# Optimization experiments

Measured on AMD Instinct MI355X. Metric: run time of the kernel, lower is better.

## Reference

```python
import jax, jax.numpy as jnp
import numpy as np

EPS = 1e-10
COMMITMENT_COST = 0.25


def setup_inputs() -> dict:
    key = jax.random.key(0)
    kx, kw = jax.random.split(key)
    B, H, W, D, K = 32, 32, 32, 256, 8192
    x = jax.random.normal(kx, (B, H, W, D), dtype=jnp.float32)
    # codebook initialized RandomUniform(-1, 1), shape [embedding_dim, n_embeddings]
    w = jax.random.uniform(kw, (D, K), dtype=jnp.float32, minval=-1.0, maxval=1.0)
    return {"x": x, "w": w, "is_training": 1}


def reference(x, w, is_training):
    D, K = w.shape
    flat_x = x.reshape(-1, D)  # [N, D]
    distances = (
        jnp.sum(flat_x * flat_x, axis=1, keepdims=True)
        - 2.0 * (flat_x @ w)
        + jnp.sum(w * w, axis=0, keepdims=True)
    )
    encoding_indices_flat = jnp.argmin(distances, axis=1)  # [N]
    encodings = jax.nn.one_hot(encoding_indices_flat, K, dtype=x.dtype)  # [N, K]
    encoding_indices = encoding_indices_flat.reshape(x.shape[:-1])  # [B, H, W]
    quantized = jnp.take(w.T, encoding_indices, axis=0)  # [B, H, W, D]

    e_latent_loss = jnp.mean((jax.lax.stop_gradient(quantized) - x) ** 2)
    q_latent_loss = jnp.mean((quantized - jax.lax.stop_gradient(x)) ** 2)
    loss = q_latent_loss + COMMITMENT_COST * e_latent_loss

    # straight-through estimator
    quantized_st = x + jax.lax.stop_gradient(quantized - x)

    avg_probs = jnp.mean(encodings, axis=0)  # [K]
    perplexity = jnp.exp(-jnp.sum(avg_probs * jnp.log(avg_probs + EPS)))

    return quantized_st, loss, perplexity, encodings, encoding_indices
```

## Files before the change

kernel.cpp:

```cpp
#include <hip/hip_runtime.h>
#include <math.h>

typedef _Float16 f16x8 __attribute__((ext_vector_type(8)));
typedef float f32x4 __attribute__((ext_vector_type(4)));

#define N_PTS 32768
#define DIM 256
#define K_CODES 8192
#define NSTRIP 4

#define WS_WNH     0
#define WS_COUNTS  32768
#define WS_LOSSP   65536
#define WS_PART    262144
#define WS_WT      2359296
#define WS_BPK     10747904

#define GLL(dst, src) __builtin_amdgcn_global_load_lds( \
    (const __attribute__((address_space(1))) void*)(src), \
    (__attribute__((address_space(3))) void*)(dst), 16, 0, 0)

__global__ void vq_prep(const float* __restrict__ w, float* __restrict__ wnh,
                        int* __restrict__ counts) {
    int k = blockIdx.x * 256 + threadIdx.x;
    double s = 0.0;
    for (int d = 0; d < DIM; ++d) {
        float v = w[(size_t)d * K_CODES + k];
        s += (double)v * (double)v;
    }
    wnh[k] = (float)(0.5 * s);
    counts[k] = 0;
}

__global__ void vq_prep_w(const float* __restrict__ w, char* __restrict__ Bpk,
                          float* __restrict__ wT) {
    __shared__ float t[64][129];
    int tid = threadIdx.x;
    int ct = blockIdx.x >> 2, ks4 = blockIdx.x & 3;
    int k0 = ks4 * 64, n0 = ct * 128;
    for (int i = 0; i < 32; ++i) {
        int idx = i * 256 + tid;
        int kk = idx >> 7, nn = idx & 127;
        t[kk][nn] = w[(size_t)(k0 + kk) * K_CODES + n0 + nn];
    }
    __syncthreads();
    for (int i = 0; i < 4; ++i) {
        int c = i * 256 + tid;
        int nn = c >> 3, k8 = c & 7;
        f16x8 hi;
#pragma unroll
        for (int e = 0; e < 8; ++e) hi[e] = (_Float16)t[k8 * 8 + e][nn];
        int off = nn * 128 + ((k8 ^ (nn & 7)) << 4);
        *(f16x8*)(Bpk + (((size_t)blockIdx.x) << 14) + off) = hi;
    }
    for (int i = 0; i < 32; ++i) {
        int idx = i * 256 + tid;
        int nn = idx >> 6, kk = idx & 63;
        wT[(size_t)(n0 + nn) * DIM + k0 + kk] = t[kk][nn];
    }
}

__global__ __launch_bounds__(256, 2)
void vq_mfma(const float* __restrict__ x, const char* __restrict__ Bpk,
             const float* __restrict__ wnh, float4* __restrict__ part) {
    __shared__ __align__(16) char Bs[2][16384];
    __shared__ float wnhs[2048];

    const int tid = threadIdx.x;
    const int lane = tid & 63;
    const int wid = tid >> 6;
    const int l15 = lane & 15, l4 = lane >> 4;
    const int mblk = blockIdx.x, strip = blockIdx.y;

    for (int i = tid; i < 2048; i += 256) wnhs[i] = wnh[strip * 2048 + i];

    f16x8 a[2][4][2];
#pragma unroll
    for (int m = 0; m < 2; ++m) {
        const float* xr = x + (size_t)(mblk * 128 + wid * 32 + m * 16 + l15) * DIM;
#pragma unroll
        for (int kp = 0; kp < 4; ++kp)
#pragma unroll
            for (int kk = 0; kk < 2; ++kk) {
                const float* p = xr + kp * 64 + (kk * 4 + l4) * 8;
                float4 u = *(const float4*)p, v = *(const float4*)(p + 4);
                f16x8 h;
                h[0] = (_Float16)u.x; h[1] = (_Float16)u.y;
                h[2] = (_Float16)u.z; h[3] = (_Float16)u.w;
                h[4] = (_Float16)v.x; h[5] = (_Float16)v.y;
                h[6] = (_Float16)v.z; h[7] = (_Float16)v.w;
                a[m][kp][kk] = h;
            }
    }

    int bB[2];
    bB[0] = l15 * 128 + ((l4 ^ (l15 & 7)) << 4);
    bB[1] = l15 * 128 + (((4 + l4) ^ (l15 & 7)) << 4);

    float v1[8], v2[8];
    int i1[8], i2[8];
#pragma unroll
    for (int r = 0; r < 8; ++r) {
        v1[r] = INFINITY; v2[r] = INFINITY;
        i1[r] = 0x7fffffff; i2[r] = 0x7fffffff;
    }

    const int t16 = tid << 4;
    const char* bbase = Bpk + (((size_t)strip * 64) << 14);

#pragma unroll
    for (int q = 0; q < 4; ++q) GLL(&Bs[0][q * 4096 + t16], bbase + q * 4096 + t16);
    __syncthreads();

    for (int ct = 0; ct < 16; ++ct) {
        f32x4 acc[2][8];
#pragma unroll
        for (int m = 0; m < 2; ++m)
#pragma unroll
            for (int n = 0; n < 8; ++n)
#pragma unroll
                for (int e = 0; e < 4; ++e) acc[m][n][e] = 0.f;

#pragma unroll
        for (int kp = 0; kp < 4; ++kp) {
            const int cur = kp & 1;
            if (ct < 15 || kp < 3) {
                const char* src = bbase + (((size_t)(ct * 4 + kp + 1)) << 14);
#pragma unroll
                for (int q = 0; q < 4; ++q)
                    GLL(&Bs[cur ^ 1][q * 4096 + t16], src + q * 4096 + t16);
            }
#pragma unroll
            for (int kk = 0; kk < 2; ++kk) {
#pragma unroll
                for (int n = 0; n < 8; ++n) {
                    f16x8 b = *(const f16x8*)(&Bs[cur][bB[kk] + n * 2048]);
                    acc[0][n] = __builtin_amdgcn_mfma_f32_16x16x32_f16(
                        a[0][kp][kk], b, acc[0][n], 0, 0, 0);
                    acc[1][n] = __builtin_amdgcn_mfma_f32_16x16x32_f16(
                        a[1][kp][kk], b, acc[1][n], 0, 0, 0);
                }
            }
            if (kp == 3) {
#pragma unroll
                for (int n = 0; n < 8; ++n) {
                    const int cl = ct * 128 + n * 16 + l15;
                    const float wv = wnhs[cl];
                    const int k = strip * 2048 + cl;
#pragma unroll
                    for (int m = 0; m < 2; ++m)
#pragma unroll
                        for (int j = 0; j < 4; ++j) {
                            const int r = m * 4 + j;
                            float v = wv - acc[m][n][j];
                            bool lt1 = v < v1[r];
                            bool lt2 = v < v2[r];
                            float tv = lt2 ? v : v2[r];
                            int ti = lt2 ? k : i2[r];
                            v2[r] = lt1 ? v1[r] : tv;
                            i2[r] = lt1 ? i1[r] : ti;
                            v1[r] = lt1 ? v : v1[r];
                            i1[r] = lt1 ? k : i1[r];
                        }
                }
            }
            __syncthreads();
        }
    }

#pragma unroll
    for (int mask = 1; mask <= 8; mask <<= 1) {
#pragma unroll
        for (int r = 0; r < 8; ++r) {
            float ov1 = __shfl_xor(v1[r], mask); int oi1 = __shfl_xor(i1[r], mask);
            float ov2 = __shfl_xor(v2[r], mask); int oi2 = __shfl_xor(i2[r], mask);
            bool fa = (v1[r] < ov1) || (v1[r] == ov1 && i1[r] < oi1);
            float nv1 = fa ? v1[r] : ov1; int ni1 = fa ? i1[r] : oi1;
            float cs = fa ? ov1 : v1[r]; int ci = fa ? oi1 : i1[r];
            float ws_ = fa ? v2[r] : ov2; int wi = fa ? i2[r] : oi2;
            bool sb = (cs < ws_) || (cs == ws_ && ci < wi);
            v1[r] = nv1; i1[r] = ni1;
            v2[r] = sb ? cs : ws_; i2[r] = sb ? ci : wi;
        }
    }
    if (l15 == 0) {
#pragma unroll
        for (int m = 0; m < 2; ++m)
#pragma unroll
            for (int j = 0; j < 4; ++j) {
                int r = m * 4 + j;
                int row = mblk * 128 + wid * 32 + m * 16 + l4 * 4 + j;
                part[(size_t)strip * N_PTS + row] =
                    make_float4(v1[r], __int_as_float(i1[r]), v2[r], __int_as_float(i2[r]));
            }
    }
}

__global__ void vq_rerank(const float4* __restrict__ part, const float* __restrict__ x,
                          const float* __restrict__ wT, int* __restrict__ counts,
                          float* __restrict__ out_idx, float* __restrict__ out_enc,
                          float* __restrict__ outq, float* __restrict__ lossPart) {
    const int lane = threadIdx.x & 63;
    const int row = blockIdx.x * 4 + (threadIdx.x >> 6);

    float v = INFINITY;
    int ii = 0x7fffffff;
    if (lane < 8) {
        float4 p = part[(size_t)(lane >> 1) * N_PTS + row];
        v = (lane & 1) ? p.z : p.x;
        ii = __float_as_int((lane & 1) ? p.w : p.y);
    }
    int sel0, sel1, sel2;
#pragma unroll
    for (int t = 0; t < 3; ++t) {
        float mv = v; int mi = ii;
#pragma unroll
        for (int mask = 1; mask <= 4; mask <<= 1) {
            float ov = __shfl_xor(mv, mask); int oi = __shfl_xor(mi, mask);
            if (ov < mv || (ov == mv && oi < mi)) { mv = ov; mi = oi; }
        }
        int win = __shfl(mi, 0);
        if (t == 0) sel0 = win; else if (t == 1) sel1 = win; else sel2 = win;
        if (ii == win) v = INFINITY;
    }
    const int grp = lane >> 4;
    int cnd = sel0;
    if (grp == 1) cnd = sel1;
    if (grp == 2) cnd = sel2;
    const int d0 = (lane & 15) * 16;
    const float* xp = x + (size_t)row * DIM + d0;
    const float* wp = wT + (size_t)cnd * DIM + d0;
    double s = 0.0;
#pragma unroll
    for (int q = 0; q < 4; ++q) {
        float4 xa = *(const float4*)(xp + q * 4);
        float4 wa = *(const float4*)(wp + q * 4);
        double dx;
        dx = (double)xa.x - (double)wa.x; s += dx * dx;
        dx = (double)xa.y - (double)wa.y; s += dx * dx;
        dx = (double)xa.z - (double)wa.z; s += dx * dx;
        dx = (double)xa.w - (double)wa.w; s += dx * dx;
    }
#pragma unroll
    for (int mask = 1; mask <= 8; mask <<= 1) s += __shfl_xor(s, mask);
    double dA = __shfl(s, 0), dB = __shfl(s, 16), dC = __shfl(s, 32);
    double bd = dA; int bi = sel0;
    if (dB < bd || (dB == bd && sel1 < bi)) { bd = dB; bi = sel1; }
    if (dC < bd || (dC == bd && sel2 < bi)) { bd = dC; bi = sel2; }
    const int best = bi;

    if (lane == 0) {
        out_idx[row] = (float)best;
        out_enc[(size_t)row * K_CODES + best] = 1.0f;
        atomicAdd(&counts[best], 1);
    }
    float4 xq = *(const float4*)(x + (size_t)row * DIM + lane * 4);
    float4 wq = *(const float4*)(wT + (size_t)best * DIM + lane * 4);
    *(float4*)(outq + (size_t)row * DIM + lane * 4) = wq;
    float d1 = wq.x - xq.x, d2 = wq.y - xq.y, d3 = wq.z - xq.z, d4 = wq.w - xq.w;
    float ls = d1 * d1 + d2 * d2 + d3 * d3 + d4 * d4;

    __shared__ float red[256];
    red[threadIdx.x] = ls;
    __syncthreads();
    for (int m = 128; m > 0; m >>= 1) {
        if (threadIdx.x < m) red[threadIdx.x] += red[threadIdx.x + m];
        __syncthreads();
    }
    if (threadIdx.x == 0) lossPart[blockIdx.x] = red[0];
}

__global__ void vq_final(const int* __restrict__ counts, const float* __restrict__ lossPart,
                         float* __restrict__ out_loss, float* __restrict__ out_perp) {
    __shared__ float red[256];
    __shared__ float red2[256];
    int tid = threadIdx.x;
    float h = 0.f;
    for (int k = tid; k < K_CODES; k += 256) {
        float p = (float)counts[k] * (1.0f / N_PTS);
        h += p * logf(p + 1e-10f);
    }
    float l = 0.f;
    for (int k = tid; k < 8192; k += 256) l += lossPart[k];
    red[tid] = h;
    red2[tid] = l;
    __syncthreads();
    for (int m = 128; m > 0; m >>= 1) {
        if (tid < m) { red[tid] += red[tid + m]; red2[tid] += red2[tid + m]; }
        __syncthreads();
    }
    if (tid == 0) {
        *out_perp = expf(-red[0]);
        *out_loss = 1.25f * red2[0] / 8388608.0f;
    }
}

extern "C" void kernel_launch(void* const* d_in, const int* in_sizes, int n_in,
                              void* d_out, int out_size, void* d_ws, size_t ws_size,
                              hipStream_t stream) {
    const float* x = (const float*)d_in[0];
    const float* w = (const float*)d_in[1];

    float* outf = (float*)d_out;
    float* outq = outf;
    float* out_loss = outf + (size_t)8388608;
    float* out_perp = outf + (size_t)8388609;
    float* out_enc = outf + (size_t)8388610;
    float* out_idx = outf + (size_t)8388610 + (size_t)268435456;

    char* wsb = (char*)d_ws;
    float* wnh = (float*)(wsb + WS_WNH);
    int* counts = (int*)(wsb + WS_COUNTS);
    float* lossPart = (float*)(wsb + WS_LOSSP);
    float4* part = (float4*)(wsb + WS_PART);
    float* wT = (float*)(wsb + WS_WT);
    char* Bpk = wsb + WS_BPK;

    vq_prep<<<dim3(32), dim3(256), 0, stream>>>(w, wnh, counts);
    vq_prep_w<<<dim3(256), dim3(256), 0, stream>>>(w, Bpk, wT);

    vq_mfma<<<dim3(256, NSTRIP), dim3(256), 0, stream>>>(x, Bpk, wnh, part);

    vq_rerank<<<dim3(8192), dim3(256), 0, stream>>>(part, x, wT, counts,
                                                    out_idx, out_enc, outq, lossPart);
    vq_final<<<dim3(1), dim3(256), 0, stream>>>(counts, lossPart, out_loss, out_perp);
}
```

Before: 246.1 us.

## Retile VQ MFMA to 2x2 warps, pack distance+index keys, rerank all candidates

Reorganizes the MFMA distance kernel so four waves form a 2x2 grid over 64-column codebook tiles. Each wave holds 64 rows of negated x fragments and seeds the accumulators with the half-norms, so the subtraction happens inside the MFMA. The top-2 tracking now packs an order-preserving float key with the 13-bit code index into one uint, which turns each compare into min/max ops, and the two column waves merge through shared memory. The B packing layout changes to 8KB chunks to match the new tiling. Rerank skips the global top-3 selection and computes exact fp64 distances for all 8 candidates in parallel. Truncating the low mantissa bits of the key may reorder close candidates, and the exact rerank is relied on to fix that.

```diff
diff --git a/kernel.cpp b/kernel.cpp
--- a/kernel.cpp
+++ b/kernel.cpp
@@ -8,6 +8,8 @@
 #define DIM 256
 #define K_CODES 8192
 #define NSTRIP 4
+#define SCOLS 2048
+#define NCT 32
 
 #define WS_WNH     0
 #define WS_COUNTS  32768
@@ -23,12 +25,16 @@
 __global__ void vq_prep(const float* __restrict__ w, float* __restrict__ wnh,
                         int* __restrict__ counts) {
     int k = blockIdx.x * 256 + threadIdx.x;
-    double s = 0.0;
-    for (int d = 0; d < DIM; ++d) {
-        float v = w[(size_t)d * K_CODES + k];
-        s += (double)v * (double)v;
-    }
-    wnh[k] = (float)(0.5 * s);
+    double s0 = 0.0, s1 = 0.0, s2 = 0.0, s3 = 0.0;
+    for (int d = 0; d < DIM; d += 4) {
+        float a = w[(size_t)d * K_CODES + k];
+        float b = w[(size_t)(d + 1) * K_CODES + k];
+        float c = w[(size_t)(d + 2) * K_CODES + k];
+        float e = w[(size_t)(d + 3) * K_CODES + k];
+        s0 += (double)a * a; s1 += (double)b * b;
+        s2 += (double)c * c; s3 += (double)e * e;
+    }
+    wnh[k] = (float)(0.5 * ((s0 + s1) + (s2 + s3)));
     counts[k] = 0;
 }
 
@@ -36,8 +42,8 @@
                           float* __restrict__ wT) {
     __shared__ float t[64][129];
     int tid = threadIdx.x;
-    int ct = blockIdx.x >> 2, ks4 = blockIdx.x & 3;
-    int k0 = ks4 * 64, n0 = ct * 128;
+    int ct128 = blockIdx.x >> 2, ks4 = blockIdx.x & 3;
+    int k0 = ks4 * 64, n0 = ct128 * 128;
     for (int i = 0; i < 32; ++i) {
         int idx = i * 256 + tid;
         int kk = idx >> 7, nn = idx & 127;
@@ -46,12 +52,17 @@
     __syncthreads();
     for (int i = 0; i < 4; ++i) {
         int c = i * 256 + tid;
-        int nn = c >> 3, k8 = c & 7;
+        int nn128 = c >> 3, k8 = c & 7;
         f16x8 hi;
 #pragma unroll
-        for (int e = 0; e < 8; ++e) hi[e] = (_Float16)t[k8 * 8 + e][nn];
-        int off = nn * 128 + ((k8 ^ (nn & 7)) << 4);
-        *(f16x8*)(Bpk + (((size_t)blockIdx.x) << 14) + off) = hi;
+        for (int e = 0; e < 8; ++e) hi[e] = (_Float16)t[k8 * 8 + e][nn128];
+        int nh = nn128 >> 6, nnl = nn128 & 63;
+        int col0 = n0 + nh * 64;
+        int strip = col0 >> 11;
+        int ctn = (col0 & 2047) >> 6;
+        size_t p = (size_t)(strip * 128 + ctn * 4 + ks4);
+        int off = nnl * 128 + ((k8 ^ (nnl & 7)) << 4);
+        *(f16x8*)(Bpk + (p << 13) + off) = hi;
     }
     for (int i = 0; i < 32; ++i) {
         int idx = i * 256 + tid;
@@ -62,105 +73,106 @@
 
 __global__ __launch_bounds__(256, 2)
 void vq_mfma(const float* __restrict__ x, const char* __restrict__ Bpk,
-             const float* __restrict__ wnh, float4* __restrict__ part) {
-    __shared__ __align__(16) char Bs[2][16384];
+             const float* __restrict__ wnh, uint2* __restrict__ part) {
+    __shared__ __align__(16) char Bs[2][8192];
     __shared__ float wnhs[2048];
+    __shared__ uint2 pmerge[128];
 
     const int tid = threadIdx.x;
     const int lane = tid & 63;
     const int wid = tid >> 6;
+    const int wr = wid >> 1, wc = wid & 1;
     const int l15 = lane & 15, l4 = lane >> 4;
     const int mblk = blockIdx.x, strip = blockIdx.y;
 
     for (int i = tid; i < 2048; i += 256) wnhs[i] = wnh[strip * 2048 + i];
 
-    f16x8 a[2][4][2];
-#pragma unroll
-    for (int m = 0; m < 2; ++m) {
-        const float* xr = x + (size_t)(mblk * 128 + wid * 32 + m * 16 + l15) * DIM;
+    f16x8 a[4][4][2];
+#pragma unroll
+    for (int m = 0; m < 4; ++m) {
+        const float* xr = x + (size_t)(mblk * 128 + wr * 64 + m * 16 + l15) * DIM;
 #pragma unroll
         for (int kp = 0; kp < 4; ++kp)
 #pragma unroll
             for (int kk = 0; kk < 2; ++kk) {
-                const float* p = xr + kp * 64 + (kk * 4 + l4) * 8;
+                const float* p = xr + kp * 64 + kk * 32 + l4 * 8;
                 float4 u = *(const float4*)p, v = *(const float4*)(p + 4);
                 f16x8 h;
-                h[0] = (_Float16)u.x; h[1] = (_Float16)u.y;
-                h[2] = (_Float16)u.z; h[3] = (_Float16)u.w;
-                h[4] = (_Float16)v.x; h[5] = (_Float16)v.y;
-                h[6] = (_Float16)v.z; h[7] = (_Float16)v.w;
+                h[0] = (_Float16)(-u.x); h[1] = (_Float16)(-u.y);
+                h[2] = (_Float16)(-u.z); h[3] = (_Float16)(-u.w);
+                h[4] = (_Float16)(-v.x); h[5] = (_Float16)(-v.y);
+                h[6] = (_Float16)(-v.z); h[7] = (_Float16)(-v.w);
                 a[m][kp][kk] = h;
             }
     }
 
-    int bB[2];
-    bB[0] = l15 * 128 + ((l4 ^ (l15 & 7)) << 4);
-    bB[1] = l15 * 128 + (((4 + l4) ^ (l15 & 7)) << 4);
-
-    float v1[8], v2[8];
-    int i1[8], i2[8];
-#pragma unroll
-    for (int r = 0; r < 8; ++r) {
-        v1[r] = INFINITY; v2[r] = INFINITY;
-        i1[r] = 0x7fffffff; i2[r] = 0x7fffffff;
-    }
+    int bb[2][2];
+#pragma unroll
+    for (int n = 0; n < 2; ++n)
+#pragma unroll
+        for (int kk = 0; kk < 2; ++kk) {
+            int nn = wc * 32 + n * 16 + l15;
+            bb[n][kk] = nn * 128 + ((((kk << 2) | l4) ^ (nn & 7)) << 4);
+        }
+
+    unsigned int v1[16], v2[16];
+#pragma unroll
+    for (int r = 0; r < 16; ++r) { v1[r] = 0xFFFFFFFFu; v2[r] = 0xFFFFFFFFu; }
 
     const int t16 = tid << 4;
-    const char* bbase = Bpk + (((size_t)strip * 64) << 14);
-
-#pragma unroll
-    for (int q = 0; q < 4; ++q) GLL(&Bs[0][q * 4096 + t16], bbase + q * 4096 + t16);
-    __syncthreads();
-
-    for (int ct = 0; ct < 16; ++ct) {
-        f32x4 acc[2][8];
-#pragma unroll
-        for (int m = 0; m < 2; ++m)
-#pragma unroll
-            for (int n = 0; n < 8; ++n)
-#pragma unroll
-                for (int e = 0; e < 4; ++e) acc[m][n][e] = 0.f;
+    const char* bbase = Bpk + ((size_t)strip << 20);
+
+    GLL(Bs[0] + t16, bbase + t16);
+    GLL(Bs[0] + 4096 + t16, bbase + 4096 + t16);
+    __syncthreads();
+
+    for (int ct = 0; ct < NCT; ++ct) {
+        f32x4 acc[4][2];
+#pragma unroll
+        for (int n = 0; n < 2; ++n) {
+            float wv = wnhs[ct * 64 + wc * 32 + n * 16 + l15];
+            f32x4 ini = {wv, wv, wv, wv};
+#pragma unroll
+            for (int m = 0; m < 4; ++m) acc[m][n] = ini;
+        }
 
 #pragma unroll
         for (int kp = 0; kp < 4; ++kp) {
             const int cur = kp & 1;
-            if (ct < 15 || kp < 3) {
-                const char* src = bbase + (((size_t)(ct * 4 + kp + 1)) << 14);
-#pragma unroll
-                for (int q = 0; q < 4; ++q)
-                    GLL(&Bs[cur ^ 1][q * 4096 + t16], src + q * 4096 + t16);
+            const int s = ct * 4 + kp;
+            if (s < 127) {
+                const char* src = bbase + ((size_t)(s + 1) << 13);
+                GLL(Bs[cur ^ 1] + t16, src + t16);
+                GLL(Bs[cur ^ 1] + 4096 + t16, src + 4096 + t16);
             }
 #pragma unroll
             for (int kk = 0; kk < 2; ++kk) {
 #pragma unroll
-                for (int n = 0; n < 8; ++n) {
-                    f16x8 b = *(const f16x8*)(&Bs[cur][bB[kk] + n * 2048]);
-                    acc[0][n] = __builtin_amdgcn_mfma_f32_16x16x32_f16(
-                        a[0][kp][kk], b, acc[0][n], 0, 0, 0);
-                    acc[1][n] = __builtin_amdgcn_mfma_f32_16x16x32_f16(
-                        a[1][kp][kk], b, acc[1][n], 0, 0, 0);
+                for (int n = 0; n < 2; ++n) {
+                    f16x8 b = *(const f16x8*)(Bs[cur] + bb[n][kk]);
+#pragma unroll
+                    for (int m = 0; m < 4; ++m)
+                        acc[m][n] = __builtin_amdgcn_mfma_f32_16x16x32_f16(
+                            a[m][kp][kk], b, acc[m][n], 0, 0, 0);
                 }
             }
             if (kp == 3) {
 #pragma unroll
-                for (int n = 0; n < 8; ++n) {
-                    const int cl = ct * 128 + n * 16 + l15;
-                    const float wv = wnhs[cl];
-                    const int k = strip * 2048 + cl;
-#pragma unroll
-                    for (int m = 0; m < 2; ++m)
+                for (int n = 0; n < 2; ++n) {
+                    const unsigned int gcol =
+                        (unsigned int)(strip * SCOLS + ct * 64 + wc * 32 + n * 16 + l15);
+#pragma unroll
+                    for (int m = 0; m < 4; ++m)
 #pragma unroll
                         for (int j = 0; j < 4; ++j) {
+                            unsigned int u = __float_as_uint(acc[m][n][j]);
+                            unsigned int key =
+                                u ^ ((unsigned int)((int)u >> 31) | 0x80000000u);
+                            key = (key & 0xFFFFE000u) | gcol;
                             const int r = m * 4 + j;
-                            float v = wv - acc[m][n][j];
-                            bool lt1 = v < v1[r];
-                            bool lt2 = v < v2[r];
-                            float tv = lt2 ? v : v2[r];
-                            int ti = lt2 ? k : i2[r];
-                            v2[r] = lt1 ? v1[r] : tv;
-                            i2[r] = lt1 ? i1[r] : ti;
-                            v1[r] = lt1 ? v : v1[r];
-                            i1[r] = lt1 ? k : i1[r];
+                            unsigned int nk = min(v1[r], key);
+                            v2[r] = min(v2[r], max(v1[r], key));
+                            v1[r] = nk;
                         }
                 }
             }
@@ -171,68 +183,55 @@
 #pragma unroll
     for (int mask = 1; mask <= 8; mask <<= 1) {
 #pragma unroll
-        for (int r = 0; r < 8; ++r) {
-            float ov1 = __shfl_xor(v1[r], mask); int oi1 = __shfl_xor(i1[r], mask);
-            float ov2 = __shfl_xor(v2[r], mask); int oi2 = __shfl_xor(i2[r], mask);
-            bool fa = (v1[r] < ov1) || (v1[r] == ov1 && i1[r] < oi1);
-            float nv1 = fa ? v1[r] : ov1; int ni1 = fa ? i1[r] : oi1;
-            float cs = fa ? ov1 : v1[r]; int ci = fa ? oi1 : i1[r];
-            float ws_ = fa ? v2[r] : ov2; int wi = fa ? i2[r] : oi2;
-            bool sb = (cs < ws_) || (cs == ws_ && ci < wi);
-            v1[r] = nv1; i1[r] = ni1;
-            v2[r] = sb ? cs : ws_; i2[r] = sb ? ci : wi;
+        for (int r = 0; r < 16; ++r) {
+            unsigned int o1 = (unsigned int)__shfl_xor((int)v1[r], mask);
+            unsigned int o2 = (unsigned int)__shfl_xor((int)v2[r], mask);
+            unsigned int n2 = min(min(v2[r], o2), max(v1[r], o1));
+            v1[r] = min(v1[r], o1);
+            v2[r] = n2;
         }
     }
-    if (l15 == 0) {
-#pragma unroll
-        for (int m = 0; m < 2; ++m)
+    if (wc == 1 && l15 == 0) {
+#pragma unroll
+        for (int m = 0; m < 4; ++m)
 #pragma unroll
             for (int j = 0; j < 4; ++j) {
                 int r = m * 4 + j;
-                int row = mblk * 128 + wid * 32 + m * 16 + l4 * 4 + j;
-                part[(size_t)strip * N_PTS + row] =
-                    make_float4(v1[r], __int_as_float(i1[r]), v2[r], __int_as_float(i2[r]));
-            }
-    }
-}
-
-__global__ void vq_rerank(const float4* __restrict__ part, const float* __restrict__ x,
+                pmerge[wr * 64 + m * 16 + l4 * 4 + j] = make_uint2(v1[r], v2[r]);
+            }
+    }
+    __syncthreads();
+    if (wc == 0 && l15 == 0) {
+#pragma unroll
+        for (int m = 0; m < 4; ++m)
+#pragma unroll
+            for (int j = 0; j < 4; ++j) {
+                int r = m * 4 + j;
+                uint2 o = pmerge[wr * 64 + m * 16 + l4 * 4 + j];
+                unsigned int n2 = min(min(v2[r], o.y), max(v1[r], o.x));
+                unsigned int n1 = min(v1[r], o.x);
+                int row = mblk * 128 + wr * 64 + m * 16 + l4 * 4 + j;
+                part[(size_t)strip * N_PTS + row] = make_uint2(n1, n2);
+            }
+    }
+}
+
+__global__ void vq_rerank(const uint2* __restrict__ part, const float* __restrict__ x,
                           const float* __restrict__ wT, int* __restrict__ counts,
                           float* __restrict__ out_idx, float* __restrict__ out_enc,
                           float* __restrict__ outq, float* __restrict__ lossPart) {
     const int lane = threadIdx.x & 63;
     const int row = blockIdx.x * 4 + (threadIdx.x >> 6);
-
-    float v = INFINITY;
-    int ii = 0x7fffffff;
-    if (lane < 8) {
-        float4 p = part[(size_t)(lane >> 1) * N_PTS + row];
-        v = (lane & 1) ? p.z : p.x;
-        ii = __float_as_int((lane & 1) ? p.w : p.y);
-    }
-    int sel0, sel1, sel2;
-#pragma unroll
-    for (int t = 0; t < 3; ++t) {
-        float mv = v; int mi = ii;
-#pragma unroll
-        for (int mask = 1; mask <= 4; mask <<= 1) {
-            float ov = __shfl_xor(mv, mask); int oi = __shfl_xor(mi, mask);
-            if (ov < mv || (ov == mv && oi < mi)) { mv = ov; mi = oi; }
-        }
-        int win = __shfl(mi, 0);
-        if (t == 0) sel0 = win; else if (t == 1) sel1 = win; else sel2 = win;
-        if (ii == win) v = INFINITY;
-    }
-    const int grp = lane >> 4;
-    int cnd = sel0;
-    if (grp == 1) cnd = sel1;
-    if (grp == 2) cnd = sel2;
-    const int d0 = (lane & 15) * 16;
+    const int c = lane >> 3;
+    uint2 pr = part[(size_t)(c >> 1) * N_PTS + row];
+    int idx = (int)(((c & 1) ? pr.y : pr.x) & 0x1FFFu);
+
+    const int d0 = (lane & 7) * 32;
     const float* xp = x + (size_t)row * DIM + d0;
-    const float* wp = wT + (size_t)cnd * DIM + d0;
+    const float* wp = wT + (size_t)idx * DIM + d0;
     double s = 0.0;
 #pragma unroll
-    for (int q = 0; q < 4; ++q) {
+    for (int q = 0; q < 8; ++q) {
         float4 xa = *(const float4*)(xp + q * 4);
         float4 wa = *(const float4*)(wp + q * 4);
         double dx;
@@ -242,11 +241,16 @@
         dx = (double)xa.w - (double)wa.w; s += dx * dx;
     }
 #pragma unroll
-    for (int mask = 1; mask <= 8; mask <<= 1) s += __shfl_xor(s, mask);
-    double dA = __shfl(s, 0), dB = __shfl(s, 16), dC = __shfl(s, 32);
-    double bd = dA; int bi = sel0;
-    if (dB < bd || (dB == bd && sel1 < bi)) { bd = dB; bi = sel1; }
-    if (dC < bd || (dC == bd && sel2 < bi)) { bd = dC; bi = sel2; }
+    for (int mask = 1; mask <= 4; mask <<= 1) s += __shfl_xor(s, mask);
+
+    double bd = __shfl(s, 0);
+    int bi = __shfl(idx, 0);
+#pragma unroll
+    for (int c2 = 1; c2 < 8; ++c2) {
+        double dc = __shfl(s, c2 * 8);
+        int ic = __shfl(idx, c2 * 8);
+        if (dc < bd || (dc == bd && ic < bi)) { bd = dc; bi = ic; }
+    }
     const int best = bi;
 
     if (lane == 0) {
@@ -312,7 +316,7 @@
     float* wnh = (float*)(wsb + WS_WNH);
     int* counts = (int*)(wsb + WS_COUNTS);
     float* lossPart = (float*)(wsb + WS_LOSSP);
-    float4* part = (float4*)(wsb + WS_PART);
+    uint2* part = (uint2*)(wsb + WS_PART);
     float* wT = (float*)(wsb + WS_WT);
     char* Bpk = wsb + WS_BPK;
 
```

After: 281.8 us. 1.15x slower.
